# Kernel tuning notes

Hardware: AMD Instinct MI355X
Metric: run time of the kernel (lower is better)

Reference implementation:

```python
import jax, jax.numpy as jnp
import numpy as np

HEADS = 8
SPLITS = 4


def setup_inputs() -> dict:
    key = jax.random.key(0)
    ks = jax.random.split(key, 5)
    B, C, N = 8, 512, 4096
    C2 = C // 2
    x = jax.random.normal(ks[0], (B, C, N), jnp.float32)
    # reduction: Conv1d(C -> C//2, k=1) => weight [C2, C], bias [C2]
    Wr = jax.random.normal(ks[1], (C2, C), jnp.float32) * (1.0 / np.sqrt(C))
    br = jnp.zeros((C2,), jnp.float32)
    # toQKV: Linear(C2 -> 3*C2, bias=False); stored as [in, out]
    Wqkv = jax.random.normal(ks[2], (C2, 3 * C2), jnp.float32) * (1.0 / np.sqrt(C2))
    # expansion: Conv1d(C2 -> C, k=1) => weight [C, C2], bias [C]
    We = jax.random.normal(ks[3], (C, C2), jnp.float32) * (1.0 / np.sqrt(C2))
    be = jnp.zeros((C,), jnp.float32)
    return {"x": x, "Wr": Wr, "br": br, "Wqkv": Wqkv, "We": We, "be": be}


def reference(x, Wr, br, Wqkv, We, be):
    B, C, N = x.shape
    h, S = HEADS, SPLITS
    # 1x1 conv reduction: [B, C, N] -> [B, C2, N]
    y = jnp.einsum('oc,bcn->bon', Wr, x) + br[None, :, None]
    t = y.transpose(0, 2, 1)                       # [B, N, C2]
    qkv = t @ Wqkv                                 # [B, N, 3*C2]
    q, k, v = jnp.split(qkv, 3, axis=-1)
    d = q.shape[-1] // h
    n = N // S

    def to_chunks(a):
        # b n (h d) -> b h S n' d  (block-diagonal chunks along the token dim)
        return a.reshape(B, N, h, d).transpose(0, 2, 1, 3).reshape(B, h, S, n, d)

    q, k, v = to_chunks(q), to_chunks(k), to_chunks(v)
    scale = d ** -0.5
    scores = jnp.einsum('bhsnd,bhsmd->bhsnm', q, k) * scale   # [B,h,S,n,n]
    attn = jax.nn.softmax(scores, axis=-1)
    o = jnp.einsum('bhsnm,bhsmd->bhsnd', attn, v)             # [B,h,S,n,d]
    # rearrange per-chunk to 'b n (h d)' and concat chunks along n (restores order)
    o = o.transpose(0, 2, 3, 1, 4).reshape(B, N, h * d)       # [B, N, C2]
    o = o.transpose(0, 2, 1)                                  # [B, C2, N]
    out = jnp.einsum('oc,bcn->bon', We, o) + be[None, :, None]  # [B, C, N]
    return out
```

## Files before the change

kernel.cpp:

```cpp
#include <hip/hip_runtime.h>
#include <hip/hip_bf16.h>

#define BATCH 8
#define CIN   512
#define NTOK  4096
#define CH    256
#define J3    768
#define NH    8
#define DH    32
#define NCH   1024

typedef _Float16 F16;
typedef _Float16 f16x8 __attribute__((ext_vector_type(8)));
typedef _Float16 f16x4 __attribute__((ext_vector_type(4)));
typedef _Float16 f16x2 __attribute__((ext_vector_type(2)));
typedef float    f32x4  __attribute__((ext_vector_type(4)));
typedef float    f32x16 __attribute__((ext_vector_type(16)));

#define QSCALE 0.25503483f


__global__ __launch_bounds__(256) void fuse_weights_kernel(
    const float* __restrict__ Wr, const float* __restrict__ br,
    const float* __restrict__ Wqkv,
    F16* __restrict__ Wc_t, float* __restrict__ bcomb)
{
    const int jb8 = blockIdx.x * 8;
    const int c = threadIdx.x;
    float acc0[8], acc1[8];
#pragma unroll
    for (int jj = 0; jj < 8; ++jj) { acc0[jj] = 0.f; acc1[jj] = 0.f; }
    for (int c2 = 0; c2 < CH; ++c2) {
        const float w0 = Wr[c2 * CIN + c];
        const float w1 = Wr[c2 * CIN + c + 256];
#pragma unroll
        for (int jj = 0; jj < 8; ++jj) {
            const float q = Wqkv[c2 * J3 + jb8 + jj];
            acc0[jj] = fmaf(w0, q, acc0[jj]);
            acc1[jj] = fmaf(w1, q, acc1[jj]);
        }
    }
    const int t0 = c >> 5, kg0 = (c >> 3) & 3, e0 = c & 7;
    const int c1 = c + 256;
    const int t1 = c1 >> 5, kg1 = (c1 >> 3) & 3, e1 = c1 & 7;
    const int jb = jb8 >> 8, row0 = jb8 & 255;
#pragma unroll
    for (int jj = 0; jj < 8; ++jj) {
        const float qs = (jb8 + jj < 256) ? QSCALE : 1.0f;
        const int row = row0 + jj;
        Wc_t[jb * 131072 + t0 * 8192 + kg0 * 2048 + row * 8 + e0] =
            (F16)(acc0[jj] * qs);
        Wc_t[jb * 131072 + t1 * 8192 + kg1 * 2048 + row * 8 + e1] =
            (F16)(acc1[jj] * qs);
    }
    if (c < 8) {
        const int j = jb8 + c;
        const float qs = (j < 256) ? QSCALE : 1.0f;
        float s = 0.f;
        for (int c2 = 0; c2 < CH; ++c2) s = fmaf(Wqkv[c2 * J3 + j], br[c2], s);
        bcomb[j] = s * qs;
    }
}

__global__ __launch_bounds__(256) void convert_we_kernel(
    const float* __restrict__ We, F16* __restrict__ We_t)
{
    const int i = blockIdx.x * 256 + threadIdx.x;
    const int j = i >> 8, c2 = i & 255;
    We_t[(j >> 7) * 32768 + (c2 >> 5) * 4096 + ((c2 >> 3) & 3) * 1024 +
         (j & 127) * 8 + (c2 & 7)] = (F16)We[i];
}

__global__ __launch_bounds__(256) void transpose_convert_kernel(
    const float* __restrict__ x, F16* __restrict__ xt_t)
{
    const int b = blockIdx.z;
    const int c0 = blockIdx.y * 8;
    const int n = blockIdx.x * 256 + threadIdx.x;

    const float* xb = x + ((size_t)b * CIN + c0) * NTOK + n;
    f16x8 v;
#pragma unroll
    for (int i = 0; i < 8; ++i)
        v[i] = (F16)xb[(size_t)i * NTOK];

    const int nb = n >> 7, row = n & 127;
    const int t = c0 >> 5, kg = (c0 >> 3) & 3;
    *(f16x8*)&xt_t[(size_t)b * 2097152 + nb * 65536 + t * 4096 + kg * 1024 +
                   row * 8] = v;
}

__global__ __launch_bounds__(512, 4) void gemm1_kernel(
    const F16* __restrict__ A,
    const F16* __restrict__ B,
    const float* __restrict__ bias,
    F16* __restrict__ Qb,
    F16* __restrict__ Kt,
    F16* __restrict__ Vt)
{
    const int b  = blockIdx.z;
    const int jb = blockIdx.y;
    const int j0 = jb * 256;
    const int nb = blockIdx.x;
    const int n0 = nb * 128;
    const int tid = threadIdx.x;
    const int w = tid >> 6, l = tid & 63;
    const int wr = w >> 1;
    const int wc = w & 1;
    const int cl = l & 15, rg = l >> 4;

    __shared__ __align__(16) char smem[49152];
    F16* Ash0 = (F16*)smem;
    F16* Ash1 = (F16*)(smem + 16384);
    F16* Bsh0 = (F16*)(smem + 32768);
    F16* Bsh1 = (F16*)(smem + 40960);
    F16* Esh  = (F16*)smem;

    f32x4 acc[4][4];
#pragma unroll
    for (int i = 0; i < 4; ++i)
#pragma unroll
        for (int j = 0; j < 4; ++j) acc[i][j] = (f32x4){0.f, 0.f, 0.f, 0.f};

    const F16* Abase = A + jb * 131072 + tid * 8;
    const F16* Bbase = B + (size_t)b * 2097152 + nb * 65536 + tid * 8;

#define G1_STAGE(Adst, Bdst, t)                                                \
    do {                                                                       \
        __builtin_amdgcn_global_load_lds(                                      \
            (const __attribute__((address_space(1))) void*)(Abase + (t) * 8192),\
            (__attribute__((address_space(3))) void*)&Adst[tid * 8], 16, 0, 0);\
        __builtin_amdgcn_global_load_lds(                                      \
            (const __attribute__((address_space(1))) void*)(Abase + (t) * 8192 \
                + 4096),                                                       \
            (__attribute__((address_space(3))) void*)&Adst[4096 + tid * 8],    \
            16, 0, 0);                                                         \
        __builtin_amdgcn_global_load_lds(                                      \
            (const __attribute__((address_space(1))) void*)(Bbase + (t) * 4096),\
            (__attribute__((address_space(3))) void*)&Bdst[tid * 8], 16, 0, 0);\
    } while (0)

    G1_STAGE(Ash0, Bsh0, 0);
    __syncthreads();

    for (int t = 0; t < 16; ++t) {
        F16* Ac = (t & 1) ? Ash1 : Ash0;
        F16* Bc = (t & 1) ? Bsh1 : Bsh0;
        if (t < 15) {
            F16* An = (t & 1) ? Ash0 : Ash1;
            F16* Bn = (t & 1) ? Bsh0 : Bsh1;
            G1_STAGE(An, Bn, t + 1);
        }
        f16x8 bf[4];
#pragma unroll
        for (int j = 0; j < 4; ++j)
            bf[j] = *(const f16x8*)&Bc[rg * 1024 + (wc * 64 + j * 16 + cl) * 8];
#pragma unroll
        for (int i = 0; i < 4; ++i) {
            const f16x8 af =
                *(const f16x8*)&Ac[rg * 2048 + (wr * 64 + i * 16 + cl) * 8];
#pragma unroll
            for (int j = 0; j < 4; ++j)
                acc[i][j] = __builtin_amdgcn_mfma_f32_16x16x32_f16(
                    af, bf[j], acc[i][j], 0, 0, 0);
        }
        __syncthreads();
    }
#undef G1_STAGE

    const int sidx = n0 >> 10;
    const int tb   = (n0 >> 6) & 15;

    if (jb < 2) {
        const size_t bN = (size_t)b * NTOK;
#pragma unroll
        for (int c = 0; c < 4; ++c) {
            if (c) __syncthreads();
            if (wc == (c >> 1)) {
#pragma unroll
                for (int i = 0; i < 4; ++i) {
#pragma unroll
                    for (int jj = 0; jj < 2; ++jj) {
                        const int jn = (c & 1) * 2 + jj;
                        const int nl = jj * 16 + cl;
                        const int jl = wr * 64 + i * 16 + rg * 4;
                        const int jg = j0 + jl;
                        f16x4 v;
#pragma unroll
                        for (int r = 0; r < 4; ++r)
                            v[r] = (F16)(acc[i][jn][r] + bias[jg + r]);
                        *(f16x4*)&Esh[nl * 264 + jl] = v;
                    }
                }
            }
            __syncthreads();
            if (jb == 0) {
                const int rr = tid >> 4, ss = tid & 15;
                const f16x8 ov0 = *(const f16x8*)&Esh[rr * 264 + ss * 16];
                const f16x8 ov1 = *(const f16x8*)&Esh[rr * 264 + ss * 16 + 8];
                F16* dst = &Qb[(bN + n0 + c * 32 + rr) * 256 + ss * 16];
                *(f16x8*)dst = ov0;
                *(f16x8*)(dst + 8) = ov1;
            } else {
                const int tloc = (tb + (c >> 1)) & 15;
#pragma unroll
                for (int p = 0; p < 2; ++p) {
                    const int uid = tid + p * 512;
                    const int nl = uid & 31, kg = (uid >> 5) & 3,
                              hh = uid >> 7;
                    const f16x8 ov =
                        *(const f16x8*)&Esh[nl * 264 + hh * 32 + kg * 8];
                    const int nk = (c & 1) * 32 + nl;
                    *(f16x8*)&Kt[(((size_t)b * NH + hh) * 4 + sidx) * 32768 +
                                 tloc * 2048 + kg * 512 + nk * 8] = ov;
                }
            }
        }
    } else {
#pragma unroll
        for (int c = 0; c < 4; ++c) {
            if (c) __syncthreads();
            if (wr == c) {
#pragma unroll
                for (int i = 0; i < 4; ++i) {
                    const int jg = j0 + c * 64 + i * 16 + rg * 4;
#pragma unroll
                    for (int jn = 0; jn < 4; ++jn) {
                        const int nl = wc * 64 + jn * 16 + cl;
#pragma unroll
                        for (int r = 0; r < 4; ++r)
                            Esh[(i * 16 + rg * 4 + r) * 136 + nl] =
                                (F16)(acc[i][jn][r] + bias[jg + r]);
                    }
                }
            }
            __syncthreads();
#pragma unroll
            for (int p = 0; p < 2; ++p) {
                const int uid = tid + p * 512;
                const int d = uid & 31, vg = (uid >> 5) & 7,
                          ttv = (uid >> 8) & 1, hl = uid >> 9;
                const int hh = c * 2 + hl;
                const int tloc = (tb + ttv) & 15;
                const f16x8 ov =
                    *(const f16x8*)&Esh[(hl * 32 + d) * 136 + ttv * 64 + vg * 8];
                *(f16x8*)&Vt[(((size_t)b * NH + hh) * 4 + sidx) * 32768 +
                             tloc * 2048 + vg * 256 + d * 8] = ov;
            }
        }
    }
}

__global__ __launch_bounds__(256) void attn_mfma_kernel(
    const F16* __restrict__ Qb,
    const F16* __restrict__ Kt,
    const F16* __restrict__ Vt,
    F16* __restrict__ O)
{
    const int bid = blockIdx.x;
    const int xcd = bid & 7, tt = bid >> 3;
    const int qb = tt & 7;
    const int pr = xcd * 32 + (tt >> 3);
    const int s = pr & 3, bh = pr >> 2;
    const int b = bh >> 3, h = bh & 7;
    const int tid = threadIdx.x;
    const int w = tid >> 6, l = tid & 63;
    const int ln = l & 31;
    const int hi = l >> 5;

    __shared__ __align__(16) F16 Klds[2][64 * 40];
    __shared__ __align__(16) F16 Vlds[2][32 * 68];

    const size_t bN = (size_t)b * NTOK + (size_t)s * NCH;
    const int q0 = qb * 128 + w * 32;

    const F16* Qp = Qb + (bN + q0 + ln) * 256 + h * DH + hi * 8;
    const f16x8 qf0 = *(const f16x8*)Qp;
    const f16x8 qf1 = *(const f16x8*)(Qp + 16);

    const F16* Kbase = Kt + (((size_t)b * NH + h) * 4 + s) * 32768 + tid * 8;
    const F16* Vbase = Vt + (((size_t)b * NH + h) * 4 + s) * 32768 + tid * 8;
    const int kw = (tid & 63) * 40 + (tid >> 6) * 8;
    const int vw = (tid & 31) * 68 + (tid >> 5) * 8;

    f16x8 kreg = *(const f16x8*)Kbase;
    f16x8 vreg = *(const f16x8*)Vbase;

    const f16x8 ones = {(F16)1.f, (F16)1.f, (F16)1.f, (F16)1.f,
                        (F16)1.f, (F16)1.f, (F16)1.f, (F16)1.f};

    f32x16 oacc = (f32x16)(0.0f);
    f32x16 lacc = (f32x16)(0.0f);

    *(f16x8*)&Klds[0][kw] = kreg;
    *(f16x4*)&Vlds[0][vw] = __builtin_shufflevector(vreg, vreg, 0, 1, 2, 3);
    *(f16x4*)&Vlds[0][vw + 4] = __builtin_shufflevector(vreg, vreg, 4, 5, 6, 7);

    for (int t = 0; t < 16; ++t) {
        const int cur = t & 1, nxt = cur ^ 1;
        __syncthreads();
        if (t < 15) {
            kreg = *(const f16x8*)(Kbase + (t + 1) * 2048);
            vreg = *(const f16x8*)(Vbase + (t + 1) * 2048);
        }
        const F16* Kb = &Klds[cur][0];
        const F16* Vb = &Vlds[cur][0];
#pragma unroll
        for (int u = 0; u < 2; ++u) {
            const int nkb = u * 32;
            const f16x8 kf0 = *(const f16x8*)&Kb[(nkb + ln) * 40 + hi * 8];
            const f16x8 kf1 = *(const f16x8*)&Kb[(nkb + ln) * 40 + 16 + hi * 8];
            f32x16 sacc = (f32x16)(0.0f);
            __builtin_amdgcn_s_setprio(1);
            sacc = __builtin_amdgcn_mfma_f32_32x32x16_f16(kf0, qf0, sacc, 0, 0, 0);
            sacc = __builtin_amdgcn_mfma_f32_32x32x16_f16(kf1, qf1, sacc, 0, 0, 0);
            __builtin_amdgcn_s_setprio(0);

            union { f16x8 v; f16x2 h[4]; } pu0, pu1;
#pragma unroll
            for (int e = 0; e < 4; ++e) {
                pu0.h[e] = __builtin_bit_cast(f16x2, __builtin_amdgcn_cvt_pkrtz(
                    __builtin_amdgcn_exp2f(sacc[2 * e]),
                    __builtin_amdgcn_exp2f(sacc[2 * e + 1])));
                pu1.h[e] = __builtin_bit_cast(f16x2, __builtin_amdgcn_cvt_pkrtz(
                    __builtin_amdgcn_exp2f(sacc[8 + 2 * e]),
                    __builtin_amdgcn_exp2f(sacc[8 + 2 * e + 1])));
            }
            const f16x8 ps = pu0.v + pu1.v;

            const int vbase = ln * 68 + nkb + 4 * hi;
            const f16x4 v00 = *(const f16x4*)&Vb[vbase];
            const f16x4 v01 = *(const f16x4*)&Vb[vbase + 8];
            const f16x4 v10 = *(const f16x4*)&Vb[vbase + 16];
            const f16x4 v11 = *(const f16x4*)&Vb[vbase + 24];
            const f16x8 vf0 = __builtin_shufflevector(v00, v01, 0, 1, 2, 3, 4, 5, 6, 7);
            const f16x8 vf1 = __builtin_shufflevector(v10, v11, 0, 1, 2, 3, 4, 5, 6, 7);

            __builtin_amdgcn_s_setprio(1);
            oacc = __builtin_amdgcn_mfma_f32_32x32x16_f16(pu0.v, vf0, oacc, 0, 0, 0);
            oacc = __builtin_amdgcn_mfma_f32_32x32x16_f16(pu1.v, vf1, oacc, 0, 0, 0);
            lacc = __builtin_amdgcn_mfma_f32_32x32x16_f16(ps, ones, lacc, 0, 0, 0);
            __builtin_amdgcn_s_setprio(0);
        }
        if (t < 15) {
            *(f16x8*)&Klds[nxt][kw] = kreg;
            *(f16x4*)&Vlds[nxt][vw] =
                __builtin_shufflevector(vreg, vreg, 0, 1, 2, 3);
            *(f16x4*)&Vlds[nxt][vw + 4] =
                __builtin_shufflevector(vreg, vreg, 4, 5, 6, 7);
        }
    }

    __syncthreads();
    F16* Elds = (F16*)&Klds[0][0] + w * 1152;
#pragma unroll
    for (int r = 0; r < 16; ++r) {
        const int qr = (r & 3) + 8 * (r >> 2) + 4 * hi;
        const float invr = __builtin_amdgcn_rcpf(lacc[r]);
        Elds[qr * 36 + ln] = (F16)(oacc[r] * invr);
    }
    __syncthreads();
    F16* Ob = O + (size_t)b * 1048576 + (s * 8 + qb) * 32768 + h * 4096;
    const int q = l & 31;
#pragma unroll
    for (int st = 0; st < 2; ++st) {
        const int kg = (l >> 5) + 2 * st;
        const f16x8 ov = *(const f16x8*)&Elds[q * 36 + kg * 8];
        *(f16x8*)&Ob[kg * 1024 + (w * 32 + q) * 8] = ov;
    }
}

__global__ __launch_bounds__(256) void gemm2_kernel(
    const F16* __restrict__ A,
    const F16* __restrict__ B,
    const float* __restrict__ bias,
    float* __restrict__ Y)
{
    const int b  = blockIdx.z;
    const int jb = blockIdx.y;
    const int j0 = jb * 128;
    const int nb = blockIdx.x;
    const int n0 = nb * 128;
    const int tid = threadIdx.x;
    const int w = tid >> 6, l = tid & 63;
    const int wr = w >> 1, wc = w & 1;
    const int cl = l & 15, rg = l >> 4;

    __shared__ __align__(16) F16 Ash[2][4096];
    __shared__ __align__(16) F16 Bsh[2][4096];

    f32x4 acc[4][4];
#pragma unroll
    for (int i = 0; i < 4; ++i)
#pragma unroll
        for (int j = 0; j < 4; ++j) acc[i][j] = (f32x4){0.f, 0.f, 0.f, 0.f};

    const int frag_off = rg * 1024 + cl * 8;
    const F16* Abase = A + jb * 32768 + tid * 8;
    const F16* Bbase = B + (size_t)b * 1048576 + nb * 32768 + tid * 8;

#define G2_STAGE(bu, t)                                                        \
    do {                                                                       \
        __builtin_amdgcn_global_load_lds(                                      \
            (const __attribute__((address_space(1))) void*)(Abase + (t) * 4096),\
            (__attribute__((address_space(3))) void*)&Ash[bu][tid * 8],        \
            16, 0, 0);                                                         \
        __builtin_amdgcn_global_load_lds(                                      \
            (const __attribute__((address_space(1))) void*)(Abase + (t) * 4096 \
                + 2048),                                                       \
            (__attribute__((address_space(3))) void*)&Ash[bu][2048 + tid * 8], \
            16, 0, 0);                                                         \
        __builtin_amdgcn_global_load_lds(                                      \
            (const __attribute__((address_space(1))) void*)(Bbase + (t) * 4096),\
            (__attribute__((address_space(3))) void*)&Bsh[bu][tid * 8],        \
            16, 0, 0);                                                         \
        __builtin_amdgcn_global_load_lds(                                      \
            (const __attribute__((address_space(1))) void*)(Bbase + (t) * 4096 \
                + 2048),                                                       \
            (__attribute__((address_space(3))) void*)&Bsh[bu][2048 + tid * 8], \
            16, 0, 0);                                                         \
    } while (0)

    G2_STAGE(0, 0);
    __syncthreads();

    for (int t = 0; t < 8; ++t) {
        const int cur = t & 1;
        if (t < 7) G2_STAGE(cur ^ 1, t + 1);

        f16x8 af[4], bfr[4];
#pragma unroll
        for (int f = 0; f < 4; ++f) {
            af[f]  = *(const f16x8*)&Ash[cur][frag_off + (wr * 64 + f * 16) * 8];
            bfr[f] = *(const f16x8*)&Bsh[cur][frag_off + (wc * 64 + f * 16) * 8];
        }
#pragma unroll
        for (int i = 0; i < 4; ++i)
#pragma unroll
            for (int j = 0; j < 4; ++j)
                acc[i][j] = __builtin_amdgcn_mfma_f32_16x16x32_f16(
                    af[i], bfr[j], acc[i][j], 0, 0, 0);
        __syncthreads();
    }
#undef G2_STAGE

#pragma unroll
    for (int i = 0; i < 4; ++i) {
        const int jj = j0 + wr * 64 + i * 16 + rg * 4;
#pragma unroll
        for (int j = 0; j < 4; ++j) {
            const int nn = n0 + wc * 64 + j * 16 + cl;
#pragma unroll
            for (int r = 0; r < 4; ++r)
                Y[((size_t)b * CIN + jj + r) * NTOK + nn] =
                    acc[i][j][r] + bias[jj + r];
        }
    }
}

extern "C" void kernel_launch(void* const* d_in, const int* in_sizes, int n_in,
                              void* d_out, int out_size, void* d_ws, size_t ws_size,
                              hipStream_t stream)
{
    const float* x    = (const float*)d_in[0];
    const float* Wr   = (const float*)d_in[1];
    const float* br   = (const float*)d_in[2];
    const float* Wqkv = (const float*)d_in[3];
    const float* We   = (const float*)d_in[4];
    const float* be   = (const float*)d_in[5];
    float* out = (float*)d_out;

    char* ws = (char*)d_ws;
    F16*   Wc    = (F16*)ws;      ws += 786432;
    float* bcomb = (float*)ws;    ws += 4096;
    F16*   We_t  = (F16*)ws;      ws += 262144;
    F16*   Qb    = (F16*)ws;      ws += (size_t)BATCH * NTOK * 256 * 2;
    F16*   Kt    = (F16*)ws;      ws += (size_t)BATCH * NH * 4 * 32768 * 2;
    F16*   Vt    = (F16*)ws;      ws += (size_t)BATCH * NH * 4 * 32768 * 2;
    F16*   xt    = (F16*)ws;
    F16*   O_t   = (F16*)ws;

    fuse_weights_kernel<<<J3 / 8, 256, 0, stream>>>(Wr, br, Wqkv, Wc, bcomb);
    convert_we_kernel<<<CIN * CH / 256, 256, 0, stream>>>(We, We_t);
    transpose_convert_kernel<<<dim3(NTOK / 256, CIN / 8, BATCH), 256, 0, stream>>>(x, xt);
    gemm1_kernel<<<dim3(NTOK / 128, J3 / 256, BATCH), 512, 0, stream>>>(
        Wc, xt, bcomb, Qb, Kt, Vt);
    attn_mfma_kernel<<<2048, 256, 0, stream>>>(Qb, Kt, Vt, O_t);
    gemm2_kernel<<<dim3(NTOK / 128, CIN / 128, BATCH), 256, 0, stream>>>(
        We_t, O_t, be, out);
}
```

Measured before the change: 179.1 us.

## Process two query tiles per wave and compute softmax row sums on VALU

```diff
diff --git a/kernel.cpp b/kernel.cpp
--- a/kernel.cpp
+++ b/kernel.cpp
@@ -251,7 +251,7 @@
     }
 }
 
-__global__ __launch_bounds__(256) void attn_mfma_kernel(
+__global__ __launch_bounds__(256, 4) void attn_mfma_kernel(
     const F16* __restrict__ Qb,
     const F16* __restrict__ Kt,
     const F16* __restrict__ Vt,
@@ -259,8 +259,8 @@
 {
     const int bid = blockIdx.x;
     const int xcd = bid & 7, tt = bid >> 3;
-    const int qb = tt & 7;
-    const int pr = xcd * 32 + (tt >> 3);
+    const int qpair = tt & 3;
+    const int pr = xcd * 32 + (tt >> 2);
     const int s = pr & 3, bh = pr >> 2;
     const int b = bh >> 3, h = bh & 7;
     const int tid = threadIdx.x;
@@ -272,11 +272,14 @@
     __shared__ __align__(16) F16 Vlds[2][32 * 68];
 
     const size_t bN = (size_t)b * NTOK + (size_t)s * NCH;
-    const int q0 = qb * 128 + w * 32;
-
-    const F16* Qp = Qb + (bN + q0 + ln) * 256 + h * DH + hi * 8;
-    const f16x8 qf0 = *(const f16x8*)Qp;
-    const f16x8 qf1 = *(const f16x8*)(Qp + 16);
+    const int q0 = qpair * 256 + w * 64;
+
+    const F16* Qpa = Qb + (bN + q0 + ln) * 256 + h * DH + hi * 8;
+    const F16* Qpb = Qpa + 32 * 256;
+    const f16x8 qfa0 = *(const f16x8*)Qpa;
+    const f16x8 qfa1 = *(const f16x8*)(Qpa + 16);
+    const f16x8 qfb0 = *(const f16x8*)Qpb;
+    const f16x8 qfb1 = *(const f16x8*)(Qpb + 16);
 
     const F16* Kbase = Kt + (((size_t)b * NH + h) * 4 + s) * 32768 + tid * 8;
     const F16* Vbase = Vt + (((size_t)b * NH + h) * 4 + s) * 32768 + tid * 8;
@@ -286,11 +289,9 @@
     f16x8 kreg = *(const f16x8*)Kbase;
     f16x8 vreg = *(const f16x8*)Vbase;
 
-    const f16x8 ones = {(F16)1.f, (F16)1.f, (F16)1.f, (F16)1.f,
-                        (F16)1.f, (F16)1.f, (F16)1.f, (F16)1.f};
-
-    f32x16 oacc = (f32x16)(0.0f);
-    f32x16 lacc = (f32x16)(0.0f);
+    f32x16 oacca = (f32x16)(0.0f);
+    f32x16 oaccb = (f32x16)(0.0f);
+    float lsum_a = 0.f, lsum_b = 0.f;
 
     *(f16x8*)&Klds[0][kw] = kreg;
     *(f16x4*)&Vlds[0][vw] = __builtin_shufflevector(vreg, vreg, 0, 1, 2, 3);
@@ -310,23 +311,49 @@
             const int nkb = u * 32;
             const f16x8 kf0 = *(const f16x8*)&Kb[(nkb + ln) * 40 + hi * 8];
             const f16x8 kf1 = *(const f16x8*)&Kb[(nkb + ln) * 40 + 16 + hi * 8];
+
             f32x16 sacc = (f32x16)(0.0f);
             __builtin_amdgcn_s_setprio(1);
-            sacc = __builtin_amdgcn_mfma_f32_32x32x16_f16(kf0, qf0, sacc, 0, 0, 0);
-            sacc = __builtin_amdgcn_mfma_f32_32x32x16_f16(kf1, qf1, sacc, 0, 0, 0);
+            sacc = __builtin_amdgcn_mfma_f32_32x32x16_f16(kf0, qfa0, sacc, 0, 0, 0);
+            sacc = __builtin_amdgcn_mfma_f32_32x32x16_f16(kf1, qfa1, sacc, 0, 0, 0);
             __builtin_amdgcn_s_setprio(0);
-
-            union { f16x8 v; f16x2 h[4]; } pu0, pu1;
+            union { f16x8 v; f16x2 h[4]; } pa0, pa1, pb0, pb1;
 #pragma unroll
             for (int e = 0; e < 4; ++e) {
-                pu0.h[e] = __builtin_bit_cast(f16x2, __builtin_amdgcn_cvt_pkrtz(
+                pa0.h[e] = __builtin_bit_cast(f16x2, __builtin_amdgcn_cvt_pkrtz(
                     __builtin_amdgcn_exp2f(sacc[2 * e]),
                     __builtin_amdgcn_exp2f(sacc[2 * e + 1])));
-                pu1.h[e] = __builtin_bit_cast(f16x2, __builtin_amdgcn_cvt_pkrtz(
+                pa1.h[e] = __builtin_bit_cast(f16x2, __builtin_amdgcn_cvt_pkrtz(
                     __builtin_amdgcn_exp2f(sacc[8 + 2 * e]),
                     __builtin_amdgcn_exp2f(sacc[8 + 2 * e + 1])));
             }
-            const f16x8 ps = pu0.v + pu1.v;
+            {
+                const f16x2 t01 = pa0.h[0] + pa0.h[1] + pa1.h[0] + pa1.h[1];
+                const f16x2 t23 = pa0.h[2] + pa0.h[3] + pa1.h[2] + pa1.h[3];
+                const f16x2 ts = t01 + t23;
+                lsum_a += (float)ts[0] + (float)ts[1];
+            }
+
+            f32x16 sb = (f32x16)(0.0f);
+            __builtin_amdgcn_s_setprio(1);
+            sb = __builtin_amdgcn_mfma_f32_32x32x16_f16(kf0, qfb0, sb, 0, 0, 0);
+            sb = __builtin_amdgcn_mfma_f32_32x32x16_f16(kf1, qfb1, sb, 0, 0, 0);
+            __builtin_amdgcn_s_setprio(0);
+#pragma unroll
+            for (int e = 0; e < 4; ++e) {
+                pb0.h[e] = __builtin_bit_cast(f16x2, __builtin_amdgcn_cvt_pkrtz(
+                    __builtin_amdgcn_exp2f(sb[2 * e]),
+                    __builtin_amdgcn_exp2f(sb[2 * e + 1])));
+                pb1.h[e] = __builtin_bit_cast(f16x2, __builtin_amdgcn_cvt_pkrtz(
+                    __builtin_amdgcn_exp2f(sb[8 + 2 * e]),
+                    __builtin_amdgcn_exp2f(sb[8 + 2 * e + 1])));
+            }
+            {
+                const f16x2 t01 = pb0.h[0] + pb0.h[1] + pb1.h[0] + pb1.h[1];
+                const f16x2 t23 = pb0.h[2] + pb0.h[3] + pb1.h[2] + pb1.h[3];
+                const f16x2 ts = t01 + t23;
+                lsum_b += (float)ts[0] + (float)ts[1];
+            }
 
             const int vbase = ln * 68 + nkb + 4 * hi;
             const f16x4 v00 = *(const f16x4*)&Vb[vbase];
@@ -337,9 +364,10 @@
             const f16x8 vf1 = __builtin_shufflevector(v10, v11, 0, 1, 2, 3, 4, 5, 6, 7);
 
             __builtin_amdgcn_s_setprio(1);
-            oacc = __builtin_amdgcn_mfma_f32_32x32x16_f16(pu0.v, vf0, oacc, 0, 0, 0);
-            oacc = __builtin_amdgcn_mfma_f32_32x32x16_f16(pu1.v, vf1, oacc, 0, 0, 0);
-            lacc = __builtin_amdgcn_mfma_f32_32x32x16_f16(ps, ones, lacc, 0, 0, 0);
+            oacca = __builtin_amdgcn_mfma_f32_32x32x16_f16(pa0.v, vf0, oacca, 0, 0, 0);
+            oacca = __builtin_amdgcn_mfma_f32_32x32x16_f16(pa1.v, vf1, oacca, 0, 0, 0);
+            oaccb = __builtin_amdgcn_mfma_f32_32x32x16_f16(pb0.v, vf0, oaccb, 0, 0, 0);
+            oaccb = __builtin_amdgcn_mfma_f32_32x32x16_f16(pb1.v, vf1, oaccb, 0, 0, 0);
             __builtin_amdgcn_s_setprio(0);
         }
         if (t < 15) {
@@ -351,22 +379,35 @@
         }
     }
 
+    lsum_a += __shfl_xor(lsum_a, 32);
+    lsum_b += __shfl_xor(lsum_b, 32);
     __syncthreads();
+    float* Ltab = (float*)&Vlds[0][0] + w * 64;
+    if (hi == 0) {
+        Ltab[ln] = lsum_a;
+        Ltab[32 + ln] = lsum_b;
+    }
     F16* Elds = (F16*)&Klds[0][0] + w * 1152;
-#pragma unroll
-    for (int r = 0; r < 16; ++r) {
-        const int qr = (r & 3) + 8 * (r >> 2) + 4 * hi;
-        const float invr = __builtin_amdgcn_rcpf(lacc[r]);
-        Elds[qr * 36 + ln] = (F16)(oacc[r] * invr);
-    }
-    __syncthreads();
-    F16* Ob = O + (size_t)b * 1048576 + (s * 8 + qb) * 32768 + h * 4096;
-    const int q = l & 31;
-#pragma unroll
-    for (int st = 0; st < 2; ++st) {
-        const int kg = (l >> 5) + 2 * st;
-        const f16x8 ov = *(const f16x8*)&Elds[q * 36 + kg * 8];
-        *(f16x8*)&Ob[kg * 1024 + (w * 32 + q) * 8] = ov;
+    const int q = ln;
+#pragma unroll
+    for (int set = 0; set < 2; ++set) {
+        const f32x16 oacc = set ? oaccb : oacca;
+#pragma unroll
+        for (int r = 0; r < 16; ++r) {
+            const int qr = (r & 3) + 8 * (r >> 2) + 4 * hi;
+            const float invr = __builtin_amdgcn_rcpf(Ltab[set * 32 + qr]);
+            Elds[qr * 36 + ln] = (F16)(oacc[r] * invr);
+        }
+        const int g = qpair * 256 + w * 64 + set * 32;
+        const int nb = s * 8 + (g >> 7);
+        const int row0 = g & 127;
+        F16* Ob = O + (size_t)b * 1048576 + nb * 32768 + h * 4096;
+#pragma unroll
+        for (int st = 0; st < 2; ++st) {
+            const int kg = hi + 2 * st;
+            const f16x8 ov = *(const f16x8*)&Elds[q * 36 + kg * 8];
+            *(f16x8*)&Ob[kg * 1024 + (row0 + q) * 8] = ov;
+        }
     }
 }
 
@@ -485,7 +526,7 @@
     transpose_convert_kernel<<<dim3(NTOK / 256, CIN / 8, BATCH), 256, 0, stream>>>(x, xt);
     gemm1_kernel<<<dim3(NTOK / 128, J3 / 256, BATCH), 512, 0, stream>>>(
         Wc, xt, bcomb, Qb, Kt, Vt);
-    attn_mfma_kernel<<<2048, 256, 0, stream>>>(Qb, Kt, Vt, O_t);
+    attn_mfma_kernel<<<1024, 256, 0, stream>>>(Qb, Kt, Vt, O_t);
     gemm2_kernel<<<dim3(NTOK / 128, CIN / 128, BATCH), 256, 0, stream>>>(
         We_t, O_t, be, out);
 }
```

New measurement: 168.0 us. 1.07x faster.
